# Kernel tuning notes

Measured on AMD Instinct MI355X. Metric: run time of the kernel, lower is better.

The kernel has to match this reference:

```python
import jax, jax.numpy as jnp
import numpy as np

N, E, DIN, H, CHID, COUT, S = 20000, 320000, 128, 4, 64, 64, 32
EPS_BN = 1e-5


def setup_inputs() -> dict:
    key = jax.random.key(0)
    ks = jax.random.split(key, 20)
    g = lambda k, shp, s=0.1: jax.random.normal(k, shp, dtype=jnp.float32) * s
    return {
        "x": jax.random.normal(ks[0], (N, DIN), dtype=jnp.float32),
        "edge_index": jax.random.randint(ks[1], (2, E), 0, N, dtype=jnp.int32),
        "struct_feat": jax.random.normal(ks[2], (N, S), dtype=jnp.float32),
        # GATConv (layer 1)
        "W1": g(ks[3], (H * CHID, DIN)),
        "att_src1": g(ks[4], (1, H, CHID)),
        "att_dst1": g(ks[5], (1, H, CHID)),
        "bias1": jnp.zeros((CHID,), jnp.float32),
        # HybridGateGATLayer (layer 2)
        "W2": g(ks[6], (H * COUT, CHID)),
        "att_src2": g(ks[7], (1, H, COUT)),
        "att_dst2": g(ks[8], (1, H, COUT)),
        "bias2": jnp.zeros((COUT,), jnp.float32),
        "Wt": g(ks[9], (1, S)),
        "bt": jnp.zeros((1,), jnp.float32),
        "We1": g(ks[10], (8, 4), 0.5),
        "be1": jnp.zeros((8,), jnp.float32),
        "We2": g(ks[11], (1, 8), 0.5),
        "be2": jnp.zeros((1,), jnp.float32),
        "betas": jnp.array([1.15, 0.85, 0.1, 0.08, 0.12], jnp.float32),
    }


def _seg_softmax(logits, seg, n):
    m = jax.ops.segment_max(logits, seg, num_segments=n)
    m = jnp.where(jnp.isfinite(m), m, 0.0)
    ex = jnp.exp(logits - m[seg])
    s = jax.ops.segment_sum(ex, seg, num_segments=n)
    return ex / (s[seg] + 1e-16)


def _cos(a, b):
    na = jnp.maximum(jnp.linalg.norm(a, axis=-1), 1e-8)
    nb = jnp.maximum(jnp.linalg.norm(b, axis=-1), 1e-8)
    return (a * b).sum(-1) / (na * nb)


def reference(x, edge_index, struct_feat, W1, att_src1, att_dst1, bias1,
              W2, att_src2, att_dst2, bias2, Wt, bt, We1, be1, We2, be2, betas):
    n = x.shape[0]
    src0, dst0 = edge_index[0], edge_index[1]
    # ---- layer 1: standard GATConv with self loops, concat=False (head mean) ----
    loop = jnp.arange(n, dtype=src0.dtype)
    src = jnp.concatenate([src0, loop])
    dst = jnp.concatenate([dst0, loop])
    h = (x @ W1.T).reshape(n, H, CHID)
    a_s = (h * att_src1).sum(-1)  # [N,H]
    a_d = (h * att_dst1).sum(-1)
    al = jax.nn.leaky_relu(a_s[src] + a_d[dst], 0.2)  # [E+N,H]
    alpha1 = _seg_softmax(al, dst, n)
    out1 = jax.ops.segment_sum(h[src] * alpha1[..., None], dst, num_segments=n)
    h1 = jax.nn.relu(out1.mean(1) + bias1)  # [N,CHID]
    # batch norm (affine=False, batch stats, biased var)
    mu = h1.mean(0)
    var = ((h1 - mu) ** 2).mean(0)
    h1 = (h1 - mu) / jnp.sqrt(var + EPS_BN)
    # ---- layer 2: HybridGateGATLayer (no self loops) ----
    x2 = (h1 @ W2.T).reshape(n, H, COUT)
    node_trust = jax.nn.sigmoid(struct_feat @ Wt.T + bt).squeeze(-1)  # [N]
    as2 = (x2 * att_src2).sum(-1)
    ad2 = (x2 * att_dst2).sum(-1)
    j, i = src0, dst0
    alpha_raw = jax.nn.leaky_relu(as2[j] + ad2[i], 0.2)  # [E,H]
    struct_sim = _cos(struct_feat[j], struct_feat[i])  # [E]
    xf = x2.reshape(n, H * COUT)
    feat_sim = _cos(xf[j], xf[i])
    agreement = struct_sim * feat_sim
    conflict = jnp.abs(struct_sim - feat_sim)
    cues = jnp.stack([struct_sim, feat_sim, agreement, conflict], axis=-1)  # [E,4]
    gate = (jax.nn.relu(cues @ We1.T + be1) @ We2.T + be2).squeeze(-1)
    edge_bonus = jax.nn.sigmoid(gate) * jax.nn.relu(agreement)
    edge_trust = jnp.sqrt(jnp.clip(node_trust[j] * node_trust[i], 0.0))
    trust_bonus = edge_trust * jax.nn.relu(0.5 * (struct_sim + feat_sim))
    gate_logit = (betas[0] * struct_sim + betas[1] * feat_sim + betas[2] * agreement
                  + betas[3] * edge_bonus + betas[4] * trust_bonus)
    alpha2 = _seg_softmax(alpha_raw + gate_logit[:, None], i, n)  # [E,H]
    out2 = jax.ops.segment_sum(x2[j] * alpha2[..., None], i, num_segments=n)
    return out2.mean(1) + bias2  # [N,COUT]
```

## Files before the change

kernel.cpp:

```cpp
#include <hip/hip_runtime.h>
#include <hip/hip_bf16.h>
#include <hip/hip_fp16.h>

#define C_DIN 128
#define C_H 4
#define C_CH 64
#define C_HC 256
#define C_S 32
#define ACH 32
#define MBLK 64

typedef __attribute__((ext_vector_type(8))) _Float16 half8;
typedef __attribute__((ext_vector_type(4))) float f32x4;

__device__ __forceinline__ float lrelu(float x) { return x >= 0.f ? x : 0.2f * x; }

__device__ __forceinline__ float sub_sum32(float v) {
#pragma unroll
    for (int off = 16; off > 0; off >>= 1) v += __shfl_xor(v, off);
    return v;
}

__global__ void k_count(const int* __restrict__ dst, int* __restrict__ deg, int E) {
    int e = blockIdx.x * blockDim.x + threadIdx.x;
    if (e < E) atomicAdd(&deg[dst[e]], 1);
}

__global__ void k_scan(const int* __restrict__ deg, int* __restrict__ row_ptr,
                       int* __restrict__ cursor, int n) {
    __shared__ int part[1024];
    int t = threadIdx.x;
    const int C = (n + 1023) / 1024;
    int base = t * C;
    int s = 0;
    for (int k = 0; k < C; ++k) {
        int idx = base + k;
        if (idx < n) s += deg[idx];
    }
    part[t] = s;
    __syncthreads();
    for (int off = 1; off < 1024; off <<= 1) {
        int v = (t >= off) ? part[t - off] : 0;
        __syncthreads();
        part[t] += v;
        __syncthreads();
    }
    int run = (t == 0) ? 0 : part[t - 1];
    for (int k = 0; k < C; ++k) {
        int idx = base + k;
        if (idx < n) { row_ptr[idx] = run; cursor[idx] = run; run += deg[idx]; }
    }
    if (t == 1023) row_ptr[n] = run;
}

__global__ void k_scatter(const int* __restrict__ src, const int* __restrict__ dst,
                          int* __restrict__ cursor, int* __restrict__ adj_src, int E) {
    int e = blockIdx.x * blockDim.x + threadIdx.x;
    if (e < E) {
        int d = dst[e];
        int p = atomicAdd(&cursor[d], 1);
        adj_src[p] = src[e];
    }
}

__global__ __launch_bounds__(256) void k_gemm1(
    const float* __restrict__ x, const float* __restrict__ W1,
    const float* __restrict__ att_s, const float* __restrict__ att_d,
    __half* __restrict__ hh_out, float* __restrict__ a_s, float* __restrict__ a_d, int n) {
    __shared__ __align__(16) _Float16 bs[4 * 16 * 64 * 8];
    __shared__ __align__(16) _Float16 as_[4 * 4 * 64 * 8];
    int t = threadIdx.x;
    int r0 = blockIdx.x * MBLK;
    {
        int c = t;
        const float4* wrow = (const float4*)(W1 + (size_t)c * C_DIN);
        int nt = c >> 4, cl = c & 15;
#pragma unroll
        for (int ch = 0; ch < 16; ++ch) {
            float4 f0 = wrow[ch * 2], f1 = wrow[ch * 2 + 1];
            int ks = ch >> 2, lg = ch & 3;
            _Float16* dst = &bs[(((ks * 16 + nt) * 64) + (lg * 16 + cl)) * 8];
            dst[0] = (_Float16)f0.x; dst[1] = (_Float16)f0.y;
            dst[2] = (_Float16)f0.z; dst[3] = (_Float16)f0.w;
            dst[4] = (_Float16)f1.x; dst[5] = (_Float16)f1.y;
            dst[6] = (_Float16)f1.z; dst[7] = (_Float16)f1.w;
        }
    }
    {
        int row = t >> 2, q = t & 3;
        int rr = r0 + row;
        int mt = row >> 4, rl = row & 15;
        const float4* xrow = (const float4*)(x + (size_t)rr * C_DIN);
#pragma unroll
        for (int cc = 0; cc < 4; ++cc) {
            int ch = q * 4 + cc;
            float4 f0 = make_float4(0, 0, 0, 0), f1 = make_float4(0, 0, 0, 0);
            if (rr < n) { f0 = xrow[ch * 2]; f1 = xrow[ch * 2 + 1]; }
            int ks = ch >> 2, lg = ch & 3;
            _Float16* dst = &as_[(((ks * 4 + mt) * 64) + (lg * 16 + rl)) * 8];
            dst[0] = (_Float16)f0.x; dst[1] = (_Float16)f0.y;
            dst[2] = (_Float16)f0.z; dst[3] = (_Float16)f0.w;
            dst[4] = (_Float16)f1.x; dst[5] = (_Float16)f1.y;
            dst[6] = (_Float16)f1.z; dst[7] = (_Float16)f1.w;
        }
    }
    __syncthreads();
    int w = t >> 6, l = t & 63;
    f32x4 acc[4][4];
#pragma unroll
    for (int mt = 0; mt < 4; ++mt)
#pragma unroll
        for (int nt = 0; nt < 4; ++nt) acc[mt][nt] = (f32x4){0.f, 0.f, 0.f, 0.f};
#pragma unroll
    for (int ks = 0; ks < 4; ++ks) {
        half8 af[4], bf[4];
#pragma unroll
        for (int mt = 0; mt < 4; ++mt)
            af[mt] = *(const half8*)&as_[(((ks * 4 + mt) * 64) + l) * 8];
#pragma unroll
        for (int nt = 0; nt < 4; ++nt)
            bf[nt] = *(const half8*)&bs[(((ks * 16 + (w * 4 + nt)) * 64) + l) * 8];
#pragma unroll
        for (int mt = 0; mt < 4; ++mt)
#pragma unroll
            for (int nt = 0; nt < 4; ++nt)
                acc[mt][nt] = __builtin_amdgcn_mfma_f32_16x16x32_f16(af[mt], bf[nt],
                                                                     acc[mt][nt], 0, 0, 0);
    }
    int cl = l & 15, rg = l >> 4;
    float atv_s[4], atv_d[4];
#pragma unroll
    for (int nt = 0; nt < 4; ++nt) {
        atv_s[nt] = att_s[w * 64 + nt * 16 + cl];
        atv_d[nt] = att_d[w * 64 + nt * 16 + cl];
    }
#pragma unroll
    for (int mt = 0; mt < 4; ++mt) {
#pragma unroll
        for (int r = 0; r < 4; ++r) {
            int rr = r0 + mt * 16 + rg * 4 + r;
            float vs = 0.f, vd = 0.f;
#pragma unroll
            for (int nt = 0; nt < 4; ++nt) {
                float v = acc[mt][nt][r];
                vs += atv_s[nt] * v;
                vd += atv_d[nt] * v;
                if (rr < n)
                    hh_out[(size_t)rr * C_HC + w * 64 + nt * 16 + cl] = __float2half(v);
            }
#pragma unroll
            for (int off = 1; off < 16; off <<= 1) {
                vs += __shfl_xor(vs, off);
                vd += __shfl_xor(vd, off);
            }
            if (cl == 0 && rr < n) { a_s[rr * C_H + w] = vs; a_d[rr * C_H + w] = vd; }
        }
    }
}

__global__ void k_layer1(const int* __restrict__ row_ptr, const int* __restrict__ adj_src,
                         const __half* __restrict__ hhlf, const float* __restrict__ a_s,
                         const float* __restrict__ a_d, const float* __restrict__ bias1,
                         float* __restrict__ h1) {
    int d = blockIdx.x;
    int t = threadIdx.x, hh = t >> 5, cp = t & 31;
    int beg = row_ptr[d], end = row_ptr[d + 1];
    float adh = a_d[d * C_H + hh];
    float p_self = expf(lrelu(a_s[d * C_H + hh] + adh));
    __shared__ float alpha_l[C_H][ACH];
    __shared__ int src_l[ACH];
    const __half2* selfrow = (const __half2*)(hhlf + (size_t)d * C_HC + hh * 64);
    float2 sv = __half22float2(selfrow[cp]);
    float accx = p_self * sv.x, accy = p_self * sv.y;
    float s_part = (cp == 0) ? p_self : 0.f;
    for (int cbeg = beg; cbeg < end; cbeg += ACH) {
        int cn = min(end - cbeg, ACH);
        __syncthreads();
        if (cp < cn) {
            int s = adj_src[cbeg + cp];
            if (hh == 0) src_l[cp] = s;
            float p = expf(lrelu(a_s[s * C_H + hh] + adh));
            alpha_l[hh][cp] = p;
            s_part += p;
        }
        __syncthreads();
        for (int i = 0; i < cn; ++i) {
            int s = src_l[i];
            float a = alpha_l[hh][i];
            float2 v = __half22float2(
                *(const __half2*)(hhlf + (size_t)s * C_HC + hh * 64 + cp * 2));
            accx += a * v.x;
            accy += a * v.y;
        }
    }
    float s = sub_sum32(s_part);
    float inv = 1.f / (s + 1e-16f);
    __shared__ float2 red[128];
    red[t] = make_float2(accx * inv, accy * inv);
    __syncthreads();
    if (t < 32) {
        float2 r0 = red[t], r1 = red[t + 32], r2 = red[t + 64], r3 = red[t + 96];
        float2 b = *(const float2*)&bias1[t * 2];
        float vx = (r0.x + r1.x + r2.x + r3.x) * 0.25f + b.x;
        float vy = (r0.y + r1.y + r2.y + r3.y) * 0.25f + b.y;
        *(float2*)&h1[(size_t)d * C_CH + t * 2] =
            make_float2(fmaxf(vx, 0.f), fmaxf(vy, 0.f));
    }
}

__global__ void k_bnstats(const float* __restrict__ h1, float* __restrict__ bn, int n) {
    int t = threadIdx.x;
    int c = t & 63, rg = t >> 6;
    float s = 0.f, s2 = 0.f;
    for (int r = blockIdx.x * 4 + rg; r < n; r += gridDim.x * 4) {
        float v = h1[(size_t)r * C_CH + c];
        s += v;
        s2 += v * v;
    }
    __shared__ float ls[256], ls2[256];
    ls[t] = s; ls2[t] = s2;
    __syncthreads();
    if (t < 64) {
        s = ls[t] + ls[t + 64] + ls[t + 128] + ls[t + 192];
        s2 = ls2[t] + ls2[t + 64] + ls2[t + 128] + ls2[t + 192];
        atomicAdd(&bn[c], s);
        atomicAdd(&bn[64 + c], s2);
    }
}

__global__ __launch_bounds__(256) void k_gemm2(
    const float* __restrict__ h1, const float* __restrict__ W2,
    const float* __restrict__ att_s, const float* __restrict__ att_d,
    const float* __restrict__ bn, __half* __restrict__ x2h,
    float* __restrict__ as2, float* __restrict__ ad2, float* __restrict__ nf, int n) {
    __shared__ __align__(16) _Float16 bs[2 * 16 * 64 * 8];
    __shared__ __align__(16) _Float16 as_[2 * 4 * 64 * 8];
    __shared__ float nq[64][4];
    int t = threadIdx.x;
    int r0 = blockIdx.x * MBLK;
    {
        int c = t;
        const float4* wrow = (const float4*)(W2 + (size_t)c * C_CH);
        int nt = c >> 4, cl = c & 15;
#pragma unroll
        for (int ch = 0; ch < 8; ++ch) {
            float4 f0 = wrow[ch * 2], f1 = wrow[ch * 2 + 1];
            int ks = ch >> 2, lg = ch & 3;
            _Float16* dst = &bs[(((ks * 16 + nt) * 64) + (lg * 16 + cl)) * 8];
            dst[0] = (_Float16)f0.x; dst[1] = (_Float16)f0.y;
            dst[2] = (_Float16)f0.z; dst[3] = (_Float16)f0.w;
            dst[4] = (_Float16)f1.x; dst[5] = (_Float16)f1.y;
            dst[6] = (_Float16)f1.z; dst[7] = (_Float16)f1.w;
        }
    }
    {
        int row = t >> 2, q = t & 3;
        int rr = r0 + row;
        int mt = row >> 4, rl = row & 15;
        const float invN = 1.f / (float)n;
        const float4* hrow = (const float4*)(h1 + (size_t)rr * C_CH);
#pragma unroll
        for (int cc = 0; cc < 2; ++cc) {
            int ch = q * 2 + cc;
            float4 f0 = make_float4(0, 0, 0, 0), f1 = make_float4(0, 0, 0, 0);
            if (rr < n) { f0 = hrow[ch * 2]; f1 = hrow[ch * 2 + 1]; }
            float4 s0 = *(const float4*)&bn[ch * 8];
            float4 s1 = *(const float4*)&bn[ch * 8 + 4];
            float4 q0 = *(const float4*)&bn[64 + ch * 8];
            float4 q1 = *(const float4*)&bn[64 + ch * 8 + 4];
            float4 mu0 = make_float4(s0.x * invN, s0.y * invN, s0.z * invN, s0.w * invN);
            float4 mu1 = make_float4(s1.x * invN, s1.y * invN, s1.z * invN, s1.w * invN);
            float4 rs0 = make_float4(rsqrtf(q0.x * invN - mu0.x * mu0.x + 1e-5f),
                                     rsqrtf(q0.y * invN - mu0.y * mu0.y + 1e-5f),
                                     rsqrtf(q0.z * invN - mu0.z * mu0.z + 1e-5f),
                                     rsqrtf(q0.w * invN - mu0.w * mu0.w + 1e-5f));
            float4 rs1 = make_float4(rsqrtf(q1.x * invN - mu1.x * mu1.x + 1e-5f),
                                     rsqrtf(q1.y * invN - mu1.y * mu1.y + 1e-5f),
                                     rsqrtf(q1.z * invN - mu1.z * mu1.z + 1e-5f),
                                     rsqrtf(q1.w * invN - mu1.w * mu1.w + 1e-5f));
            int ks = ch >> 2, lg = ch & 3;
            _Float16* dst = &as_[(((ks * 4 + mt) * 64) + (lg * 16 + rl)) * 8];
            dst[0] = (_Float16)((f0.x - mu0.x) * rs0.x);
            dst[1] = (_Float16)((f0.y - mu0.y) * rs0.y);
            dst[2] = (_Float16)((f0.z - mu0.z) * rs0.z);
            dst[3] = (_Float16)((f0.w - mu0.w) * rs0.w);
            dst[4] = (_Float16)((f1.x - mu1.x) * rs1.x);
            dst[5] = (_Float16)((f1.y - mu1.y) * rs1.y);
            dst[6] = (_Float16)((f1.z - mu1.z) * rs1.z);
            dst[7] = (_Float16)((f1.w - mu1.w) * rs1.w);
        }
    }
    __syncthreads();
    int w = t >> 6, l = t & 63;
    f32x4 acc[4][4];
#pragma unroll
    for (int mt = 0; mt < 4; ++mt)
#pragma unroll
        for (int nt = 0; nt < 4; ++nt) acc[mt][nt] = (f32x4){0.f, 0.f, 0.f, 0.f};
#pragma unroll
    for (int ks = 0; ks < 2; ++ks) {
        half8 af[4], bf[4];
#pragma unroll
        for (int mt = 0; mt < 4; ++mt)
            af[mt] = *(const half8*)&as_[(((ks * 4 + mt) * 64) + l) * 8];
#pragma unroll
        for (int nt = 0; nt < 4; ++nt)
            bf[nt] = *(const half8*)&bs[(((ks * 16 + (w * 4 + nt)) * 64) + l) * 8];
#pragma unroll
        for (int mt = 0; mt < 4; ++mt)
#pragma unroll
            for (int nt = 0; nt < 4; ++nt)
                acc[mt][nt] = __builtin_amdgcn_mfma_f32_16x16x32_f16(af[mt], bf[nt],
                                                                     acc[mt][nt], 0, 0, 0);
    }
    int cl = l & 15, rg = l >> 4;
    float atv_s[4], atv_d[4];
#pragma unroll
    for (int nt = 0; nt < 4; ++nt) {
        atv_s[nt] = att_s[w * 64 + nt * 16 + cl];
        atv_d[nt] = att_d[w * 64 + nt * 16 + cl];
    }
#pragma unroll
    for (int mt = 0; mt < 4; ++mt) {
#pragma unroll
        for (int r = 0; r < 4; ++r) {
            int rr = r0 + mt * 16 + rg * 4 + r;
            float vs = 0.f, vd = 0.f, vq = 0.f;
#pragma unroll
            for (int nt = 0; nt < 4; ++nt) {
                float v = acc[mt][nt][r];
                vs += atv_s[nt] * v;
                vd += atv_d[nt] * v;
                vq += v * v;
                if (rr < n)
                    x2h[(size_t)rr * C_HC + w * 64 + nt * 16 + cl] = __float2half(v);
            }
#pragma unroll
            for (int off = 1; off < 16; off <<= 1) {
                vs += __shfl_xor(vs, off);
                vd += __shfl_xor(vd, off);
                vq += __shfl_xor(vq, off);
            }
            if (cl == 0 && rr < n) {
                as2[rr * C_H + w] = vs;
                ad2[rr * C_H + w] = vd;
                nq[mt * 16 + rg * 4 + r][w] = vq;
            }
        }
    }
    __syncthreads();
    if (t < MBLK) {
        int rr = r0 + t;
        if (rr < n) {
            float qq = nq[t][0] + nq[t][1] + nq[t][2] + nq[t][3];
            nf[rr] = fmaxf(sqrtf(qq), 1e-8f);
        }
    }
}

__global__ void k_trust(const float* __restrict__ sf, const float* __restrict__ Wt,
                        const float* __restrict__ bt, float* __restrict__ trust,
                        float* __restrict__ ns, int n) {
    int i = blockIdx.x * blockDim.x + threadIdx.x;
    if (i >= n) return;
    const float4* r4 = (const float4*)(sf + (size_t)i * C_S);
    const float4* w4 = (const float4*)Wt;
    float d = 0.f, q = 0.f;
#pragma unroll
    for (int k = 0; k < 8; ++k) {
        float4 a = r4[k], w = w4[k];
        d += a.x * w.x + a.y * w.y + a.z * w.z + a.w * w.w;
        q += a.x * a.x + a.y * a.y + a.z * a.z + a.w * a.w;
    }
    trust[i] = 1.f / (1.f + expf(-(d + bt[0])));
    ns[i] = fmaxf(sqrtf(q), 1e-8f);
}

__global__ __launch_bounds__(128) void k_fused2(
    const int* __restrict__ row_ptr, const int* __restrict__ adj_src,
    const float* __restrict__ sf, const __half* __restrict__ x2h,
    const float* __restrict__ ns, const float* __restrict__ nf,
    const float* __restrict__ trust, const float* __restrict__ as2,
    const float* __restrict__ ad2, const float* __restrict__ We1,
    const float* __restrict__ be1, const float* __restrict__ We2,
    const float* __restrict__ be2, const float* __restrict__ betas,
    const float* __restrict__ bias2, float* __restrict__ out) {
    __shared__ int js[ACH];
    __shared__ float pbuf[C_H][ACH];
    __shared__ float2 red[128];
    int d = blockIdx.x;
    int t = threadIdx.x, hh = t >> 5, cp = t & 31;
    int er = t >> 2, q = t & 3;
    int beg = row_ptr[d], end = row_ptr[d + 1];
    float4 xdreg[8], sfdreg[2];
    {
        const float4* dr = (const float4*)(x2h + (size_t)d * C_HC + q * 64);
#pragma unroll
        for (int u = 0; u < 8; ++u) xdreg[u] = dr[u];
        const float4* sr = (const float4*)(sf + (size_t)d * C_S + q * 8);
        sfdreg[0] = sr[0]; sfdreg[1] = sr[1];
    }
    float4 ad2d = *(const float4*)&ad2[d * C_H];
    float nsd = ns[d], nfd = nf[d], trd = trust[d];
    float accx = 0.f, accy = 0.f, s_part = 0.f;
    for (int cbeg = beg; cbeg < end; cbeg += ACH) {
        int cn = min(end - cbeg, ACH);
        __syncthreads();
        if (q == 0 && er < cn) js[er] = adj_src[cbeg + er];
        __syncthreads();
        float fd = 0.f, sd = 0.f;
        int j = 0;
        if (er < cn) {
            j = js[er];
            const float4* grow = (const float4*)(x2h + (size_t)j * C_HC + q * 64);
#pragma unroll
            for (int u = 0; u < 8; ++u) {
                float4 a4 = grow[u];
                const __half2* pa = (const __half2*)&a4;
                const __half2* pb = (const __half2*)&xdreg[u];
#pragma unroll
                for (int k = 0; k < 4; ++k) {
                    float2 a = __half22float2(pa[k]), b = __half22float2(pb[k]);
                    fd += a.x * b.x + a.y * b.y;
                }
            }
            const float4* sj = (const float4*)(sf + (size_t)j * C_S + q * 8);
#pragma unroll
            for (int u = 0; u < 2; ++u) {
                float4 a = sj[u], b = sfdreg[u];
                sd += a.x * b.x + a.y * b.y + a.z * b.z + a.w * b.w;
            }
        }
        fd += __shfl_xor(fd, 1); fd += __shfl_xor(fd, 2);
        sd += __shfl_xor(sd, 1); sd += __shfl_xor(sd, 2);
        if (q == 0 && er < cn) {
            float ss = sd / (nsd * ns[j]);
            float fs = fd / (nfd * nf[j]);
            float agr = ss * fs;
            float con = fabsf(ss - fs);
            float gate = be2[0];
#pragma unroll
            for (int o = 0; o < 8; ++o) {
                float hdn = We1[o * 4 + 0] * ss + We1[o * 4 + 1] * fs +
                            We1[o * 4 + 2] * agr + We1[o * 4 + 3] * con + be1[o];
                gate += We2[o] * fmaxf(hdn, 0.f);
            }
            float eb = (1.f / (1.f + expf(-gate))) * fmaxf(agr, 0.f);
            float et = sqrtf(fmaxf(trd * trust[j], 0.f));
            float tb = et * fmaxf(0.5f * (ss + fs), 0.f);
            float g = betas[0] * ss + betas[1] * fs + betas[2] * agr +
                      betas[3] * eb + betas[4] * tb;
            float4 asj = *(const float4*)&as2[j * C_H];
            pbuf[0][er] = expf(lrelu(asj.x + ad2d.x) + g);
            pbuf[1][er] = expf(lrelu(asj.y + ad2d.y) + g);
            pbuf[2][er] = expf(lrelu(asj.z + ad2d.z) + g);
            pbuf[3][er] = expf(lrelu(asj.w + ad2d.w) + g);
        }
        __syncthreads();
        for (int i = 0; i < cn; ++i) {
            int jj = js[i];
            float pv = pbuf[hh][i];
            float2 v = __half22float2(
                *(const __half2*)(x2h + (size_t)jj * C_HC + hh * 64 + cp * 2));
            accx += pv * v.x;
            accy += pv * v.y;
        }
        if (cp < cn) s_part += pbuf[hh][cp];
    }
    float s = sub_sum32(s_part);
    float inv = 1.f / (s + 1e-16f);
    red[t] = make_float2(accx * inv, accy * inv);
    __syncthreads();
    if (t < 32) {
        float2 r0 = red[t], r1 = red[t + 32], r2 = red[t + 64], r3 = red[t + 96];
        float2 b = *(const float2*)&bias2[t * 2];
        float vx = (r0.x + r1.x + r2.x + r3.x) * 0.25f + b.x;
        float vy = (r0.y + r1.y + r2.y + r3.y) * 0.25f + b.y;
        *(float2*)&out[(size_t)d * C_CH + t * 2] = make_float2(vx, vy);
    }
}

static inline size_t al256(size_t x) { return (x + 255) & ~(size_t)255; }

extern "C" void kernel_launch(void* const* d_in, const int* in_sizes, int n_in,
                              void* d_out, int out_size, void* d_ws, size_t ws_size,
                              hipStream_t stream) {
    const float* x      = (const float*)d_in[0];
    const int*   ei     = (const int*)d_in[1];
    const float* sf     = (const float*)d_in[2];
    const float* W1     = (const float*)d_in[3];
    const float* atts1  = (const float*)d_in[4];
    const float* attd1  = (const float*)d_in[5];
    const float* bias1  = (const float*)d_in[6];
    const float* W2     = (const float*)d_in[7];
    const float* atts2  = (const float*)d_in[8];
    const float* attd2  = (const float*)d_in[9];
    const float* bias2  = (const float*)d_in[10];
    const float* Wt     = (const float*)d_in[11];
    const float* bt     = (const float*)d_in[12];
    const float* We1    = (const float*)d_in[13];
    const float* be1    = (const float*)d_in[14];
    const float* We2    = (const float*)d_in[15];
    const float* be2    = (const float*)d_in[16];
    const float* betas  = (const float*)d_in[17];

    const int N = in_sizes[0] / C_DIN;
    const int E = in_sizes[1] / 2;
    const int* srcs = ei;
    const int* dsts = ei + E;

    char* p = (char*)d_ws;
    size_t off = 0;
    auto take = [&](size_t bytes) { char* r = p + off; off = al256(off + bytes); return r; };
    __half* hhlf  = (__half*)take((size_t)N * C_HC * 2);
    float* h1     = (float*)take((size_t)N * C_CH * 4);
    float* a_s1   = (float*)take((size_t)N * C_H * 4);
    float* a_d1   = (float*)take((size_t)N * C_H * 4);
    float* nf     = (float*)take((size_t)N * 4);
    float* ns     = (float*)take((size_t)N * 4);
    float* trust  = (float*)take((size_t)N * 4);
    int*   deg    = (int*)take((size_t)N * 4);
    int*   rowp   = (int*)take((size_t)(N + 1) * 4);
    int*   cursor = (int*)take((size_t)N * 4);
    int*   adj_s  = (int*)take((size_t)E * 4);
    float* bn     = (float*)take(128 * 4);
    (void)ws_size;
    __half* x2h = hhlf;
    float* as2  = a_s1;
    float* ad2  = a_d1;

    hipMemsetAsync(deg, 0, (size_t)N * 4, stream);
    hipMemsetAsync(bn, 0, 128 * 4, stream);

    k_count<<<(E + 255) / 256, 256, 0, stream>>>(dsts, deg, E);
    k_scan<<<1, 1024, 0, stream>>>(deg, rowp, cursor, N);
    k_scatter<<<(E + 255) / 256, 256, 0, stream>>>(srcs, dsts, cursor, adj_s, E);

    k_gemm1<<<(N + MBLK - 1) / MBLK, 256, 0, stream>>>(x, W1, atts1, attd1, hhlf, a_s1, a_d1, N);
    k_layer1<<<N, 128, 0, stream>>>(rowp, adj_s, hhlf, a_s1, a_d1, bias1, h1);
    k_bnstats<<<128, 256, 0, stream>>>(h1, bn, N);

    k_gemm2<<<(N + MBLK - 1) / MBLK, 256, 0, stream>>>(h1, W2, atts2, attd2, bn, x2h,
                                                       as2, ad2, nf, N);
    k_trust<<<(N + 255) / 256, 256, 0, stream>>>(sf, Wt, bt, trust, ns, N);
    k_fused2<<<N, 128, 0, stream>>>(rowp, adj_s, sf, x2h, ns, nf, trust, as2, ad2,
                                    We1, be1, We2, be2, betas, bias2, (float*)d_out);
}
```

Baseline: 340.5 us.

## Pre-swizzle weights to fp16 once and stage neighbor rows in LDS for layer 2

Adds a small kernel that converts W1 and W2 to fp16 in the MFMA fragment layout once per call, so the GEMM kernels read B fragments directly from global memory instead of having every block convert and stage the weights in shared memory. In the fused layer-2 kernel, each neighbor row of x2h is loaded once per wavefront into an LDS buffer and reused for both the cosine dot products and the weighted aggregation, which removes the second global gather. This adds an extra launch and more LDS per block (about 17 KB). The direct global B-fragment reads depend on the cache.

```diff
diff --git a/kernel.cpp b/kernel.cpp
--- a/kernel.cpp
+++ b/kernel.cpp
@@ -9,6 +9,7 @@
 #define C_S 32
 #define ACH 32
 #define MBLK 64
+#define XROW 264
 
 typedef __attribute__((ext_vector_type(8))) _Float16 half8;
 typedef __attribute__((ext_vector_type(4))) float f32x4;
@@ -63,29 +64,42 @@
     }
 }
 
+__global__ void k_prepw(const float* __restrict__ W1, const float* __restrict__ W2,
+                        _Float16* __restrict__ W1f, _Float16* __restrict__ W2f) {
+    int i = blockIdx.x * blockDim.x + threadIdx.x;
+    if (i < 4096) {
+        int ks = i >> 10, rem = i & 1023, nt = rem >> 6, lpos = rem & 63;
+        int c = nt * 16 + (lpos & 15);
+        int kb = (ks * 4 + (lpos >> 4)) * 8;
+        const float4* src = (const float4*)(W1 + (size_t)c * C_DIN + kb);
+        float4 f0 = src[0], f1 = src[1];
+        _Float16* dst = &W1f[(size_t)i * 8];
+        dst[0] = (_Float16)f0.x; dst[1] = (_Float16)f0.y;
+        dst[2] = (_Float16)f0.z; dst[3] = (_Float16)f0.w;
+        dst[4] = (_Float16)f1.x; dst[5] = (_Float16)f1.y;
+        dst[6] = (_Float16)f1.z; dst[7] = (_Float16)f1.w;
+    } else if (i < 4096 + 2048) {
+        int ii = i - 4096;
+        int ks = ii >> 10, rem = ii & 1023, nt = rem >> 6, lpos = rem & 63;
+        int c = nt * 16 + (lpos & 15);
+        int kb = (ks * 4 + (lpos >> 4)) * 8;
+        const float4* src = (const float4*)(W2 + (size_t)c * C_CH + kb);
+        float4 f0 = src[0], f1 = src[1];
+        _Float16* dst = &W2f[(size_t)ii * 8];
+        dst[0] = (_Float16)f0.x; dst[1] = (_Float16)f0.y;
+        dst[2] = (_Float16)f0.z; dst[3] = (_Float16)f0.w;
+        dst[4] = (_Float16)f1.x; dst[5] = (_Float16)f1.y;
+        dst[6] = (_Float16)f1.z; dst[7] = (_Float16)f1.w;
+    }
+}
+
 __global__ __launch_bounds__(256) void k_gemm1(
-    const float* __restrict__ x, const float* __restrict__ W1,
+    const float* __restrict__ x, const _Float16* __restrict__ W1f,
     const float* __restrict__ att_s, const float* __restrict__ att_d,
     __half* __restrict__ hh_out, float* __restrict__ a_s, float* __restrict__ a_d, int n) {
-    __shared__ __align__(16) _Float16 bs[4 * 16 * 64 * 8];
     __shared__ __align__(16) _Float16 as_[4 * 4 * 64 * 8];
     int t = threadIdx.x;
     int r0 = blockIdx.x * MBLK;
-    {
-        int c = t;
-        const float4* wrow = (const float4*)(W1 + (size_t)c * C_DIN);
-        int nt = c >> 4, cl = c & 15;
-#pragma unroll
-        for (int ch = 0; ch < 16; ++ch) {
-            float4 f0 = wrow[ch * 2], f1 = wrow[ch * 2 + 1];
-            int ks = ch >> 2, lg = ch & 3;
-            _Float16* dst = &bs[(((ks * 16 + nt) * 64) + (lg * 16 + cl)) * 8];
-            dst[0] = (_Float16)f0.x; dst[1] = (_Float16)f0.y;
-            dst[2] = (_Float16)f0.z; dst[3] = (_Float16)f0.w;
-            dst[4] = (_Float16)f1.x; dst[5] = (_Float16)f1.y;
-            dst[6] = (_Float16)f1.z; dst[7] = (_Float16)f1.w;
-        }
-    }
     {
         int row = t >> 2, q = t & 3;
         int rr = r0 + row;
@@ -106,6 +120,7 @@
     }
     __syncthreads();
     int w = t >> 6, l = t & 63;
+    const half8* Wv = (const half8*)W1f;
     f32x4 acc[4][4];
 #pragma unroll
     for (int mt = 0; mt < 4; ++mt)
@@ -119,7 +134,7 @@
             af[mt] = *(const half8*)&as_[(((ks * 4 + mt) * 64) + l) * 8];
 #pragma unroll
         for (int nt = 0; nt < 4; ++nt)
-            bf[nt] = *(const half8*)&bs[(((ks * 16 + (w * 4 + nt)) * 64) + l) * 8];
+            bf[nt] = Wv[((ks * 16 + (w * 4 + nt)) * 64) + l];
 #pragma unroll
         for (int mt = 0; mt < 4; ++mt)
 #pragma unroll
@@ -229,30 +244,14 @@
 }
 
 __global__ __launch_bounds__(256) void k_gemm2(
-    const float* __restrict__ h1, const float* __restrict__ W2,
+    const float* __restrict__ h1, const _Float16* __restrict__ W2f,
     const float* __restrict__ att_s, const float* __restrict__ att_d,
     const float* __restrict__ bn, __half* __restrict__ x2h,
     float* __restrict__ as2, float* __restrict__ ad2, float* __restrict__ nf, int n) {
-    __shared__ __align__(16) _Float16 bs[2 * 16 * 64 * 8];
     __shared__ __align__(16) _Float16 as_[2 * 4 * 64 * 8];
     __shared__ float nq[64][4];
     int t = threadIdx.x;
     int r0 = blockIdx.x * MBLK;
-    {
-        int c = t;
-        const float4* wrow = (const float4*)(W2 + (size_t)c * C_CH);
-        int nt = c >> 4, cl = c & 15;
-#pragma unroll
-        for (int ch = 0; ch < 8; ++ch) {
-            float4 f0 = wrow[ch * 2], f1 = wrow[ch * 2 + 1];
-            int ks = ch >> 2, lg = ch & 3;
-            _Float16* dst = &bs[(((ks * 16 + nt) * 64) + (lg * 16 + cl)) * 8];
-            dst[0] = (_Float16)f0.x; dst[1] = (_Float16)f0.y;
-            dst[2] = (_Float16)f0.z; dst[3] = (_Float16)f0.w;
-            dst[4] = (_Float16)f1.x; dst[5] = (_Float16)f1.y;
-            dst[6] = (_Float16)f1.z; dst[7] = (_Float16)f1.w;
-        }
-    }
     {
         int row = t >> 2, q = t & 3;
         int rr = r0 + row;
@@ -292,6 +291,7 @@
     }
     __syncthreads();
     int w = t >> 6, l = t & 63;
+    const half8* Wv = (const half8*)W2f;
     f32x4 acc[4][4];
 #pragma unroll
     for (int mt = 0; mt < 4; ++mt)
@@ -305,7 +305,7 @@
             af[mt] = *(const half8*)&as_[(((ks * 4 + mt) * 64) + l) * 8];
 #pragma unroll
         for (int nt = 0; nt < 4; ++nt)
-            bf[nt] = *(const half8*)&bs[(((ks * 16 + (w * 4 + nt)) * 64) + l) * 8];
+            bf[nt] = Wv[((ks * 16 + (w * 4 + nt)) * 64) + l];
 #pragma unroll
         for (int mt = 0; mt < 4; ++mt)
 #pragma unroll
@@ -385,57 +385,49 @@
     const float* __restrict__ be1, const float* __restrict__ We2,
     const float* __restrict__ be2, const float* __restrict__ betas,
     const float* __restrict__ bias2, float* __restrict__ out) {
+    __shared__ __align__(16) _Float16 xr[ACH * XROW];
     __shared__ int js[ACH];
+    __shared__ float fdL[ACH], sdL[ACH];
     __shared__ float pbuf[C_H][ACH];
     __shared__ float2 red[128];
     int d = blockIdx.x;
     int t = threadIdx.x, hh = t >> 5, cp = t & 31;
-    int er = t >> 2, q = t & 3;
     int beg = row_ptr[d], end = row_ptr[d + 1];
-    float4 xdreg[8], sfdreg[2];
-    {
-        const float4* dr = (const float4*)(x2h + (size_t)d * C_HC + q * 64);
-#pragma unroll
-        for (int u = 0; u < 8; ++u) xdreg[u] = dr[u];
-        const float4* sr = (const float4*)(sf + (size_t)d * C_S + q * 8);
-        sfdreg[0] = sr[0]; sfdreg[1] = sr[1];
-    }
+    float4 xd4 = ((const float4*)(x2h + (size_t)d * C_HC))[cp];
+    float sfdl = sf[(size_t)d * C_S + cp];
     float4 ad2d = *(const float4*)&ad2[d * C_H];
     float nsd = ns[d], nfd = nf[d], trd = trust[d];
     float accx = 0.f, accy = 0.f, s_part = 0.f;
     for (int cbeg = beg; cbeg < end; cbeg += ACH) {
         int cn = min(end - cbeg, ACH);
         __syncthreads();
-        if (q == 0 && er < cn) js[er] = adj_src[cbeg + er];
-        __syncthreads();
-        float fd = 0.f, sd = 0.f;
-        int j = 0;
-        if (er < cn) {
-            j = js[er];
-            const float4* grow = (const float4*)(x2h + (size_t)j * C_HC + q * 64);
-#pragma unroll
-            for (int u = 0; u < 8; ++u) {
-                float4 a4 = grow[u];
-                const __half2* pa = (const __half2*)&a4;
-                const __half2* pb = (const __half2*)&xdreg[u];
-#pragma unroll
-                for (int k = 0; k < 4; ++k) {
-                    float2 a = __half22float2(pa[k]), b = __half22float2(pb[k]);
-                    fd += a.x * b.x + a.y * b.y;
-                }
-            }
-            const float4* sj = (const float4*)(sf + (size_t)j * C_S + q * 8);
-#pragma unroll
-            for (int u = 0; u < 2; ++u) {
-                float4 a = sj[u], b = sfdreg[u];
-                sd += a.x * b.x + a.y * b.y + a.z * b.z + a.w * b.w;
-            }
-        }
-        fd += __shfl_xor(fd, 1); fd += __shfl_xor(fd, 2);
-        sd += __shfl_xor(sd, 1); sd += __shfl_xor(sd, 2);
-        if (q == 0 && er < cn) {
-            float ss = sd / (nsd * ns[j]);
-            float fs = fd / (nfd * nf[j]);
+        if (t < cn) js[t] = adj_src[cbeg + t];
+        __syncthreads();
+        for (int r = hh; r < cn; r += 4) {
+            int j = js[r];
+            float4 v4 = ((const float4*)(x2h + (size_t)j * C_HC))[cp];
+            ((float4*)&xr[(size_t)r * XROW])[cp] = v4;
+            float fdp = 0.f;
+            const __half2* pa = (const __half2*)&v4;
+            const __half2* pb = (const __half2*)&xd4;
+#pragma unroll
+            for (int k = 0; k < 4; ++k) {
+                float2 a = __half22float2(pa[k]), b = __half22float2(pb[k]);
+                fdp += a.x * b.x + a.y * b.y;
+            }
+            float sdp = sf[(size_t)j * C_S + cp] * sfdl;
+#pragma unroll
+            for (int off = 16; off > 0; off >>= 1) {
+                fdp += __shfl_xor(fdp, off);
+                sdp += __shfl_xor(sdp, off);
+            }
+            if (cp == 0) { fdL[r] = fdp; sdL[r] = sdp; }
+        }
+        __syncthreads();
+        if (t < cn) {
+            int j = js[t];
+            float ss = sdL[t] / (nsd * ns[j]);
+            float fs = fdL[t] / (nfd * nf[j]);
             float agr = ss * fs;
             float con = fabsf(ss - fs);
             float gate = be2[0];
@@ -451,17 +443,16 @@
             float g = betas[0] * ss + betas[1] * fs + betas[2] * agr +
                       betas[3] * eb + betas[4] * tb;
             float4 asj = *(const float4*)&as2[j * C_H];
-            pbuf[0][er] = expf(lrelu(asj.x + ad2d.x) + g);
-            pbuf[1][er] = expf(lrelu(asj.y + ad2d.y) + g);
-            pbuf[2][er] = expf(lrelu(asj.z + ad2d.z) + g);
-            pbuf[3][er] = expf(lrelu(asj.w + ad2d.w) + g);
+            pbuf[0][t] = expf(lrelu(asj.x + ad2d.x) + g);
+            pbuf[1][t] = expf(lrelu(asj.y + ad2d.y) + g);
+            pbuf[2][t] = expf(lrelu(asj.z + ad2d.z) + g);
+            pbuf[3][t] = expf(lrelu(asj.w + ad2d.w) + g);
         }
         __syncthreads();
         for (int i = 0; i < cn; ++i) {
-            int jj = js[i];
             float pv = pbuf[hh][i];
             float2 v = __half22float2(
-                *(const __half2*)(x2h + (size_t)jj * C_HC + hh * 64 + cp * 2));
+                *(const __half2*)&xr[(size_t)i * XROW + hh * 64 + cp * 2]);
             accx += pv * v.x;
             accy += pv * v.y;
         }
@@ -523,6 +514,8 @@
     int*   rowp   = (int*)take((size_t)(N + 1) * 4);
     int*   cursor = (int*)take((size_t)N * 4);
     int*   adj_s  = (int*)take((size_t)E * 4);
+    _Float16* W1f = (_Float16*)take(4096 * 8 * 2);
+    _Float16* W2f = (_Float16*)take(2048 * 8 * 2);
     float* bn     = (float*)take(128 * 4);
     (void)ws_size;
     __half* x2h = hhlf;
@@ -532,15 +525,17 @@
     hipMemsetAsync(deg, 0, (size_t)N * 4, stream);
     hipMemsetAsync(bn, 0, 128 * 4, stream);
 
+    k_prepw<<<24, 256, 0, stream>>>(W1, W2, W1f, W2f);
     k_count<<<(E + 255) / 256, 256, 0, stream>>>(dsts, deg, E);
     k_scan<<<1, 1024, 0, stream>>>(deg, rowp, cursor, N);
     k_scatter<<<(E + 255) / 256, 256, 0, stream>>>(srcs, dsts, cursor, adj_s, E);
 
-    k_gemm1<<<(N + MBLK - 1) / MBLK, 256, 0, stream>>>(x, W1, atts1, attd1, hhlf, a_s1, a_d1, N);
+    k_gemm1<<<(N + MBLK - 1) / MBLK, 256, 0, stream>>>(x, W1f, atts1, attd1, hhlf, a_s1,
+                                                       a_d1, N);
     k_layer1<<<N, 128, 0, stream>>>(rowp, adj_s, hhlf, a_s1, a_d1, bias1, h1);
     k_bnstats<<<128, 256, 0, stream>>>(h1, bn, N);
 
-    k_gemm2<<<(N + MBLK - 1) / MBLK, 256, 0, stream>>>(h1, W2, atts2, attd2, bn, x2h,
+    k_gemm2<<<(N + MBLK - 1) / MBLK, 256, 0, stream>>>(h1, W2f, atts2, attd2, bn, x2h,
                                                        as2, ad2, nf, N);
     k_trust<<<(N + 255) / 256, 256, 0, stream>>>(sf, Wt, bt, trust, ns, N);
     k_fused2<<<N, 128, 0, stream>>>(rowp, adj_s, sf, x2h, ns, nf, trust, as2, ad2,
```

New measurement: 307.4 us. -9.7%, faster.
